# Kernel optimization log

Measured on AMD Instinct MI355X. Metric: run time of the kernel, lower is better.

The kernel has to match this reference:

```python
import jax, jax.numpy as jnp
import numpy as np

RSQRT2 = 2 ** (-0.5)
B, S, D_IN = 2, 4096, 1024
H, D_HEAD = 8, 64            # num_heads, attention_dim (per-head qk and v dim)
QK_DIM = H * D_HEAD          # 512
V_DIM = H * D_HEAD           # 512
OUT_DIM = D_IN               # 1024 (output_dim defaults to input_dim)
LN_EPS = 1e-5


def setup_inputs() -> dict:
    key = jax.random.key(0)
    ks = jax.random.split(key, 8)
    def lecun(k, fan_in, shape):
        return jax.random.normal(k, shape, dtype=jnp.float32) * (1.0 / np.sqrt(fan_in))
    return {
        "x": jax.random.normal(ks[0], (B, S, D_IN), dtype=jnp.float32),
        # weights stored [in, out] (transposed torch Linear layout)
        "W_qk": lecun(ks[1], D_IN, (D_IN, 2 * QK_DIM)),
        "b_qk": jnp.zeros((2 * QK_DIM,), jnp.float32),
        "W_v": lecun(ks[2], D_IN, (D_IN, V_DIM)),
        "b_v": jnp.zeros((V_DIM,), jnp.float32),
        "W_out": lecun(ks[3], V_DIM, (V_DIM, OUT_DIM)),
        "b_out": jnp.zeros((OUT_DIM,), jnp.float32),
        "ln_gamma": jnp.ones((OUT_DIM,), jnp.float32),
        "ln_beta": jnp.zeros((OUT_DIM,), jnp.float32),
    }


def _layernorm(y, gamma, beta):
    mu = jnp.mean(y, axis=-1, keepdims=True)
    var = jnp.mean(jnp.square(y - mu), axis=-1, keepdims=True)
    return (y - mu) * jax.lax.rsqrt(var + LN_EPS) * gamma + beta


def reference(x, W_qk, b_qk, W_v, b_v, W_out, b_out, ln_gamma, ln_beta):
    b, s, _ = x.shape
    scale = D_HEAD ** (-0.5)
    qk = x @ W_qk + b_qk                          # [b, s, 2*h*d]
    qk = qk.reshape(b, s, H, D_HEAD, 2)           # c (q/k) is fastest axis
    q, k = qk[..., 0], qk[..., 1]                 # [b, s, h, d]
    v = (x @ W_v + b_v).reshape(b, s, H, D_HEAD)  # [b, s, h, d]
    # manual multi-head attention, full O(s^2) score matrix (as in source)
    sim = jnp.einsum("bihd,bjhd->bhij", q, k) * scale
    attn = jax.nn.softmax(sim, axis=-1)           # [b, h, i, j]
    o = jnp.einsum("bhij,bjhd->bihd", attn, v)    # [b, s, h, d]
    o = o.reshape(b, s, V_DIM)                    # 'b h s d -> b s (h d)'
    y = _layernorm(o @ W_out + b_out, ln_gamma, ln_beta)
    return (y + x) * RSQRT2
```

## Files before the change

kernel.cpp:

```cpp
#include <hip/hip_runtime.h>
#include <stdint.h>

typedef short bf16x8 __attribute__((ext_vector_type(8)));
typedef float f32x4 __attribute__((ext_vector_type(4)));
typedef unsigned short ushort_t;

#define RSQRT2_F 0.70710678118654752440f
#define QSCALE_F 0.18033688011114382f

__device__ __forceinline__ ushort_t f2bf(float f) {
  union { float f; uint32_t u; } c; c.f = f;
  uint32_t u = c.u;
  uint32_t r = (u + 0x7fffu + ((u >> 16) & 1u)) >> 16;
  return (ushort_t)r;
}
__device__ __forceinline__ float bf2f(ushort_t u) {
  union { uint32_t u; float f; } c; c.u = ((uint32_t)u) << 16;
  return c.f;
}
__device__ __forceinline__ uint32_t fbits(float f) {
  union { float f; uint32_t u; } c; c.f = f; return c.u;
}

__device__ __forceinline__ void gload_lds16(const void* g, void* l) {
  __builtin_amdgcn_global_load_lds(
      (const __attribute__((address_space(1))) void*)g,
      (__attribute__((address_space(3))) void*)l, 16, 0, 0);
}

__global__ __launch_bounds__(256) void k_cvt_x(const float* __restrict__ x,
                                               ushort_t* __restrict__ xb) {
  int i = (blockIdx.x * 256 + threadIdx.x) * 4;
  float4 f = *(const float4*)(x + i);
  ushort4 o;
  o.x = f2bf(f.x); o.y = f2bf(f.y); o.z = f2bf(f.z); o.w = f2bf(f.w);
  *(ushort4*)(xb + i) = o;
}

__global__ __launch_bounds__(256) void k_build_wqkv(const float* __restrict__ Wqk,
                                                    const float* __restrict__ bqk,
                                                    const float* __restrict__ Wv,
                                                    const float* __restrict__ bv,
                                                    ushort_t* __restrict__ Wt,
                                                    float* __restrict__ biasAll) {
  int k = blockIdx.x * 256 + threadIdx.x;
  int n = blockIdx.y;
  float w, bb;
  if (n < 512)       { w = Wqk[(size_t)k * 1024 + 2 * n] * QSCALE_F;     bb = bqk[2 * n] * QSCALE_F; }
  else if (n < 1024) { w = Wqk[(size_t)k * 1024 + 2 * (n - 512) + 1];    bb = bqk[2 * (n - 512) + 1]; }
  else               { w = Wv[(size_t)k * 512 + (n - 1024)];             bb = bv[n - 1024]; }
  Wt[(size_t)n * 1024 + k] = f2bf(w);
  if (k == 0) biasAll[n] = bb;
}

__global__ __launch_bounds__(256) void k_build_wout(const float* __restrict__ Wout,
                                                    ushort_t* __restrict__ Wt) {
  int k = blockIdx.x * 256 + threadIdx.x;
  int n = blockIdx.y;
  Wt[(size_t)n * 512 + k] = f2bf(Wout[(size_t)k * 1024 + n]);
}

template <int MODE>
__global__ __launch_bounds__(256) void k_gemm_bt(
    const ushort_t* __restrict__ A, const ushort_t* __restrict__ Bt,
    const float* __restrict__ bias,
    ushort_t* __restrict__ out0, ushort_t* __restrict__ out1, ushort_t* __restrict__ out2,
    int M, int N, int K) {
  __shared__ __align__(16) ushort_t As[2][4][128][8];
  __shared__ __align__(16) ushort_t Bs[2][4][128][8];
  const int t = threadIdx.x;
  const int lane = t & 63;
  const int wave = t >> 6;

  const int nby = N >> 7;
  const int nwg = gridDim.x;
  const int xcd = blockIdx.x & 7, pos = blockIdx.x >> 3;
  const int swz = xcd * (nwg >> 3) + pos;
  const int bx = swz / nby, by = swz % nby;
  const int m0 = bx * 128, n0 = by * 128;

  const int wm = (wave >> 1) * 64, wn = (wave & 1) * 64;
  const int lg = lane >> 4, lr = lane & 15;

  const int srow = t & 127, sg = t >> 7;
  const ushort_t* gA = A + (size_t)(m0 + srow) * K + sg * 8;
  const ushort_t* gB = Bt + (size_t)(n0 + srow) * K + sg * 8;

  f32x4 acc[4][4] = {};

#define GEMM_STAGE(k0, bsel)                                   \
  do {                                                         \
    gload_lds16(gA + (k0), &As[bsel][sg][srow][0]);            \
    gload_lds16(gA + (k0) + 16, &As[bsel][sg + 2][srow][0]);   \
    gload_lds16(gB + (k0), &Bs[bsel][sg][srow][0]);            \
    gload_lds16(gB + (k0) + 16, &Bs[bsel][sg + 2][srow][0]);   \
  } while (0)

  GEMM_STAGE(0, 0);
  __syncthreads();
  int buf = 0;
  for (int k0 = 0; k0 < K; k0 += 32) {
    if (k0 + 32 < K) GEMM_STAGE(k0 + 32, buf ^ 1);
    bf16x8 af[4], bfr[4];
#pragma unroll
    for (int mi = 0; mi < 4; mi++) af[mi] = *(const bf16x8*)&As[buf][lg][wm + mi * 16 + lr][0];
#pragma unroll
    for (int ni = 0; ni < 4; ni++) bfr[ni] = *(const bf16x8*)&Bs[buf][lg][wn + ni * 16 + lr][0];
#pragma unroll
    for (int mi = 0; mi < 4; mi++)
#pragma unroll
      for (int ni = 0; ni < 4; ni++)
        acc[mi][ni] = __builtin_amdgcn_mfma_f32_16x16x32_bf16(af[mi], bfr[ni], acc[mi][ni], 0, 0, 0);
    __syncthreads();
    buf ^= 1;
  }
#undef GEMM_STAGE

#pragma unroll
  for (int mi = 0; mi < 4; mi++) {
    int rowb = m0 + wm + mi * 16 + (lane >> 4) * 4;
#pragma unroll
    for (int ni = 0; ni < 4; ni++) {
      int col = n0 + wn + ni * 16 + lr;
      float bc = bias[col];
#pragma unroll
      for (int reg = 0; reg < 4; reg++) {
        int row = rowb + reg;
        float v = acc[mi][ni][reg] + bc;
        if (MODE == 0) {
          if (col < 512) {
            out0[(size_t)row * 512 + col] = f2bf(v);
          } else if (col < 1024) {
            out1[(size_t)row * 512 + (col - 512)] = f2bf(v);
          } else {
            int hd = col - 1024;
            int bb = row >> 12, s = row & 4095;
            out2[((size_t)(bb << 9) + hd) * 4096 + s] = f2bf(v);
          }
        } else {
          out0[(size_t)row * 1024 + col] = f2bf(v);
        }
      }
    }
  }
}

__global__ __launch_bounds__(256, 2) void k_attn(const ushort_t* __restrict__ Qb,
                                                 const ushort_t* __restrict__ Kb,
                                                 const ushort_t* __restrict__ Vt,
                                                 ushort_t* __restrict__ Opart,
                                                 float* __restrict__ lpart) {
  __shared__ __align__(16) ushort_t Ks[2][8][64][8];
  __shared__ __align__(16) ushort_t Vs[2][8][64][8];
  __shared__ __align__(16) ushort_t Pl[4][4][1024];
  const int S = 4096;
  const int t = threadIdx.x, lane = t & 63, wave = t >> 6;
  const int lg = lane >> 4, lr = lane & 15;

  const int bid = blockIdx.x;
  const int xcd = bid & 7, idx = bid >> 3;
  const int bh = (xcd << 1) | (idx >> 5);
  const int rem = idx & 31;
  const int qb = rem >> 1;
  const int half = rem & 1;
  const int b = bh >> 3, h = bh & 7;
  const int qbase = qb * 256 + wave * 64;
  const int kvbase = half * 2048;

  bf16x8 qf[4][2];
#pragma unroll
  for (int su = 0; su < 4; su++) {
    const ushort_t* qp = Qb + ((size_t)(b * S + qbase + su * 16 + lr)) * 512 + h * 64 + lg * 8;
    qf[su][0] = *(const bf16x8*)qp;
    qf[su][1] = *(const bf16x8*)(qp + 32);
  }

  const int cj = t & 63, cg = t >> 6;
  const ushort_t* gK = Kb + ((size_t)b * S + cj) * 512 + h * 64 + cg * 8;
  const ushort_t* gV = Vt + ((size_t)bh * 64 + cj) * 4096 + cg * 8;

  const bf16x8 vones = {(short)0x3F80, (short)0x3F80, (short)0x3F80, (short)0x3F80,
                        (short)0x3F80, (short)0x3F80, (short)0x3F80, (short)0x3F80};

  int poff[4], pread[2];
#pragma unroll
  for (int nt = 0; nt < 4; nt++) poff[nt] = (lr * 128 + nt * 32 + lg * 8) ^ ((lr & 7) << 4);
#pragma unroll
  for (int kc = 0; kc < 2; kc++) pread[kc] = (lr * 128 + kc * 64 + lg * 16) ^ ((lr & 7) << 4);

  f32x4 of[4][4] = {};
  f32x4 of_sum[4] = {};

#define ATTN_STAGE(kv0, bsel)                                         \
  do {                                                                \
    gload_lds16(gK + (size_t)(kv0) * 512, &Ks[bsel][cg][cj][0]);      \
    gload_lds16(gK + (size_t)(kv0) * 512 + 32, &Ks[bsel][cg + 4][cj][0]); \
    gload_lds16(gV + (kv0), &Vs[bsel][cg][cj][0]);                    \
    gload_lds16(gV + (kv0) + 32, &Vs[bsel][cg + 4][cj][0]);           \
  } while (0)

  ATTN_STAGE(kvbase, 0);
  __syncthreads();
  int buf = 0;

  for (int kv0 = kvbase; kv0 < kvbase + 2048; kv0 += 64) {
    if (kv0 + 64 < kvbase + 2048) ATTN_STAGE(kv0 + 64, buf ^ 1);

    f32x4 sf[4][4];
    __builtin_amdgcn_s_setprio(1);
#pragma unroll
    for (int nt = 0; nt < 4; nt++) {
      bf16x8 kf0 = *(const bf16x8*)&Ks[buf][lg][nt * 16 + lr][0];
      bf16x8 kf1 = *(const bf16x8*)&Ks[buf][4 + lg][nt * 16 + lr][0];
#pragma unroll
      for (int su = 0; su < 4; su++) {
        f32x4 z = {};
        z = __builtin_amdgcn_mfma_f32_16x16x32_bf16(kf0, qf[su][0], z, 0, 0, 0);
        sf[su][nt] = __builtin_amdgcn_mfma_f32_16x16x32_bf16(kf1, qf[su][1], z, 0, 0, 0);
      }
    }
    __builtin_amdgcn_s_setprio(0);

    bf16x8 pf[4][2];
#pragma unroll
    for (int su = 0; su < 4; su++) {
      char* Pb = (char*)&Pl[wave][su][0];
#pragma unroll
      for (int nt = 0; nt < 4; nt++) {
        float p0 = __builtin_amdgcn_exp2f(sf[su][nt][0]);
        float p1 = __builtin_amdgcn_exp2f(sf[su][nt][1]);
        float p2 = __builtin_amdgcn_exp2f(sf[su][nt][2]);
        float p3 = __builtin_amdgcn_exp2f(sf[su][nt][3]);
        uint32_t w0 = (fbits(p0) >> 16) | (fbits(p1) & 0xffff0000u);
        uint32_t w1 = (fbits(p2) >> 16) | (fbits(p3) & 0xffff0000u);
        *(uint2*)(Pb + poff[nt]) = make_uint2(w0, w1);
      }
#pragma unroll
      for (int kc = 0; kc < 2; kc++) pf[su][kc] = *(const bf16x8*)(Pb + pread[kc]);
    }

    __builtin_amdgcn_s_setprio(1);
#pragma unroll
    for (int dt = 0; dt < 4; dt++) {
      bf16x8 vf0 = *(const bf16x8*)&Vs[buf][lg][dt * 16 + lr][0];
      bf16x8 vf1 = *(const bf16x8*)&Vs[buf][4 + lg][dt * 16 + lr][0];
#pragma unroll
      for (int su = 0; su < 4; su++) {
        of[su][dt] = __builtin_amdgcn_mfma_f32_16x16x32_bf16(pf[su][0], vf0, of[su][dt], 0, 0, 0);
        of[su][dt] = __builtin_amdgcn_mfma_f32_16x16x32_bf16(pf[su][1], vf1, of[su][dt], 0, 0, 0);
      }
    }
#pragma unroll
    for (int su = 0; su < 4; su++) {
      of_sum[su] = __builtin_amdgcn_mfma_f32_16x16x32_bf16(pf[su][0], vones, of_sum[su], 0, 0, 0);
      of_sum[su] = __builtin_amdgcn_mfma_f32_16x16x32_bf16(pf[su][1], vones, of_sum[su], 0, 0, 0);
    }
    __builtin_amdgcn_s_setprio(0);

    __syncthreads();
    buf ^= 1;
  }
#undef ATTN_STAGE

  ushort_t* Opw = Opart + ((size_t)half * 8192 + (size_t)b * 4096) * 512;
#pragma unroll
  for (int su = 0; su < 4; su++) {
#pragma unroll
    for (int dt = 0; dt < 4; dt++)
#pragma unroll
      for (int r = 0; r < 4; r++) {
        int q = qbase + su * 16 + lg * 4 + r;
        Opw[(size_t)q * 512 + h * 64 + dt * 16 + lr] = f2bf(of[su][dt][r]);
      }
    if (lr == 0) {
#pragma unroll
      for (int r = 0; r < 4; r++) {
        int q = qbase + su * 16 + lg * 4 + r;
        lpart[(((size_t)half * 2 + b) * 8 + h) * 4096 + q] = of_sum[su][r];
      }
    }
  }
}

__global__ __launch_bounds__(128) void k_merge(const ushort_t* __restrict__ Opart,
                                               const float* __restrict__ lpart,
                                               ushort_t* __restrict__ Ob) {
  const int row = blockIdx.x;
  const int t = threadIdx.x;
  const int col = t * 4;
  const int b = row >> 12, q = row & 4095;
  const int h = col >> 6;
  float l = lpart[(((size_t)0 * 2 + b) * 8 + h) * 4096 + q] +
            lpart[(((size_t)1 * 2 + b) * 8 + h) * 4096 + q];
  float inv = 1.0f / l;
  ushort4 a = *(const ushort4*)(Opart + (size_t)row * 512 + col);
  ushort4 c = *(const ushort4*)(Opart + ((size_t)8192 + row) * 512 + col);
  ushort4 o;
  o.x = f2bf((bf2f(a.x) + bf2f(c.x)) * inv);
  o.y = f2bf((bf2f(a.y) + bf2f(c.y)) * inv);
  o.z = f2bf((bf2f(a.z) + bf2f(c.z)) * inv);
  o.w = f2bf((bf2f(a.w) + bf2f(c.w)) * inv);
  *(ushort4*)(Ob + (size_t)row * 512 + col) = o;
}

__global__ __launch_bounds__(256) void k_ln(const ushort_t* __restrict__ ypre,
                                            const float* __restrict__ x,
                                            const float* __restrict__ gamma,
                                            const float* __restrict__ beta,
                                            float* __restrict__ out) {
  __shared__ float red[8];
  const int row = blockIdx.x, t = threadIdx.x;
  const ushort_t* yr = ypre + (size_t)row * 1024;
  ushort4 u = *(const ushort4*)(yr + t * 4);
  float v0 = bf2f(u.x), v1 = bf2f(u.y), v2 = bf2f(u.z), v3 = bf2f(u.w);
  float s = v0 + v1 + v2 + v3;
  float sq = v0 * v0 + v1 * v1 + v2 * v2 + v3 * v3;
#pragma unroll
  for (int m = 32; m; m >>= 1) { s += __shfl_xor(s, m, 64); sq += __shfl_xor(sq, m, 64); }
  if ((t & 63) == 0) { red[t >> 6] = s; red[4 + (t >> 6)] = sq; }
  __syncthreads();
  s = red[0] + red[1] + red[2] + red[3];
  sq = red[4] + red[5] + red[6] + red[7];
  float mu = s * (1.f / 1024.f);
  float var = sq * (1.f / 1024.f) - mu * mu;
  float inv = rsqrtf(var + 1e-5f);
  int c = t * 4;
  float4 xf = *(const float4*)(x + (size_t)row * 1024 + c);
  float4 o;
  o.x = ((v0 - mu) * inv * gamma[c + 0] + beta[c + 0] + xf.x) * RSQRT2_F;
  o.y = ((v1 - mu) * inv * gamma[c + 1] + beta[c + 1] + xf.y) * RSQRT2_F;
  o.z = ((v2 - mu) * inv * gamma[c + 2] + beta[c + 2] + xf.z) * RSQRT2_F;
  o.w = ((v3 - mu) * inv * gamma[c + 3] + beta[c + 3] + xf.w) * RSQRT2_F;
  *(float4*)(out + (size_t)row * 1024 + c) = o;
}

extern "C" void kernel_launch(void* const* d_in, const int* in_sizes, int n_in,
                              void* d_out, int out_size, void* d_ws, size_t ws_size,
                              hipStream_t stream) {
  (void)in_sizes; (void)n_in; (void)out_size; (void)ws_size;
  const float* x     = (const float*)d_in[0];
  const float* Wqk   = (const float*)d_in[1];
  const float* bqk   = (const float*)d_in[2];
  const float* Wv    = (const float*)d_in[3];
  const float* bv    = (const float*)d_in[4];
  const float* Wout  = (const float*)d_in[5];
  const float* bout  = (const float*)d_in[6];
  const float* gamma = (const float*)d_in[7];
  const float* beta  = (const float*)d_in[8];
  float* out = (float*)d_out;

  char* ws = (char*)d_ws;
  size_t off = 0;
  auto alloc = [&](size_t bytes) {
    off = (off + 255) & ~(size_t)255;
    void* p = ws + off;
    off += bytes;
    return p;
  };
  ushort_t* xb    = (ushort_t*)alloc(8192ull * 1024 * 2);
  ushort_t* Wqkvt = (ushort_t*)alloc(1536ull * 1024 * 2);
  float*    biasA = (float*)   alloc(1536ull * 4);
  ushort_t* Woutt = (ushort_t*)alloc(1024ull * 512 * 2);
  ushort_t* Qb    = (ushort_t*)alloc(8192ull * 512 * 2);
  ushort_t* Kbuf  = (ushort_t*)alloc(8192ull * 512 * 2);
  ushort_t* Vtb   = (ushort_t*)alloc(1024ull * 4096 * 2);
  ushort_t* Ob    = (ushort_t*)alloc(8192ull * 512 * 2);
  float*    lpart = (float*)   alloc(2ull * 2 * 8 * 4096 * 4);
  ushort_t* Opart = xb;
  ushort_t* ypre  = xb;

  k_cvt_x<<<8192, 256, 0, stream>>>(x, xb);
  k_build_wqkv<<<dim3(4, 1536), 256, 0, stream>>>(Wqk, bqk, Wv, bv, Wqkvt, biasA);
  k_build_wout<<<dim3(2, 1024), 256, 0, stream>>>(Wout, Woutt);
  k_gemm_bt<0><<<768, 256, 0, stream>>>(xb, Wqkvt, biasA, Qb, Kbuf, Vtb, 8192, 1536, 1024);
  k_attn<<<512, 256, 0, stream>>>(Qb, Kbuf, Vtb, Opart, lpart);
  k_merge<<<8192, 128, 0, stream>>>(Opart, lpart, Ob);
  k_gemm_bt<1><<<512, 256, 0, stream>>>(Ob, Woutt, bout, ypre, nullptr, nullptr, 8192, 1024, 512);
  k_ln<<<8192, 256, 0, stream>>>(ypre, x, gamma, beta, out);
}
```

Measured before the change: 207.3 us.

## Split attention KV range into quarters and raise occupancy to four blocks

The attention kernel now splits each query block's KV range into four 1024-key quarters instead of two halves, doubling the grid to 1024 blocks. The P staging buffer in LDS is shrunk to one slice per wave, and launch bounds ask for four blocks per CU. The merge kernel now sums four partial outputs and four row-sum partials, and buffers are reused to hold the extra partials. The goal is more parallelism and occupancy on the attention stage. In exchange, partial-output traffic and merge work double, and register pressure may rise under the tighter launch bound.

```diff
diff --git a/kernel.cpp b/kernel.cpp
--- a/kernel.cpp
+++ b/kernel.cpp
@@ -145,27 +145,30 @@
   }
 }
 
-__global__ __launch_bounds__(256, 2) void k_attn(const ushort_t* __restrict__ Qb,
+__global__ __launch_bounds__(256, 4) void k_attn(const ushort_t* __restrict__ Qb,
                                                  const ushort_t* __restrict__ Kb,
                                                  const ushort_t* __restrict__ Vt,
-                                                 ushort_t* __restrict__ Opart,
+                                                 ushort_t* __restrict__ O0,
+                                                 ushort_t* __restrict__ O1,
+                                                 ushort_t* __restrict__ O2,
+                                                 ushort_t* __restrict__ O3,
                                                  float* __restrict__ lpart) {
   __shared__ __align__(16) ushort_t Ks[2][8][64][8];
   __shared__ __align__(16) ushort_t Vs[2][8][64][8];
-  __shared__ __align__(16) ushort_t Pl[4][4][1024];
+  __shared__ __align__(16) ushort_t Pl[4][1024];
   const int S = 4096;
   const int t = threadIdx.x, lane = t & 63, wave = t >> 6;
   const int lg = lane >> 4, lr = lane & 15;
 
   const int bid = blockIdx.x;
   const int xcd = bid & 7, idx = bid >> 3;
-  const int bh = (xcd << 1) | (idx >> 5);
-  const int rem = idx & 31;
-  const int qb = rem >> 1;
-  const int half = rem & 1;
+  const int bh = (xcd << 1) | (idx >> 6);
+  const int rem = idx & 63;
+  const int qb = rem >> 2;
+  const int quarter = rem & 3;
   const int b = bh >> 3, h = bh & 7;
   const int qbase = qb * 256 + wave * 64;
-  const int kvbase = half * 2048;
+  const int kvbase = quarter * 1024;
 
   bf16x8 qf[4][2];
 #pragma unroll
@@ -203,8 +206,8 @@
   __syncthreads();
   int buf = 0;
 
-  for (int kv0 = kvbase; kv0 < kvbase + 2048; kv0 += 64) {
-    if (kv0 + 64 < kvbase + 2048) ATTN_STAGE(kv0 + 64, buf ^ 1);
+  for (int kv0 = kvbase; kv0 < kvbase + 1024; kv0 += 64) {
+    if (kv0 + 64 < kvbase + 1024) ATTN_STAGE(kv0 + 64, buf ^ 1);
 
     f32x4 sf[4][4];
     __builtin_amdgcn_s_setprio(1);
@@ -224,7 +227,7 @@
     bf16x8 pf[4][2];
 #pragma unroll
     for (int su = 0; su < 4; su++) {
-      char* Pb = (char*)&Pl[wave][su][0];
+      char* Pb = (char*)&Pl[wave][0];
 #pragma unroll
       for (int nt = 0; nt < 4; nt++) {
         float p0 = __builtin_amdgcn_exp2f(sf[su][nt][0]);
@@ -262,7 +265,8 @@
   }
 #undef ATTN_STAGE
 
-  ushort_t* Opw = Opart + ((size_t)half * 8192 + (size_t)b * 4096) * 512;
+  ushort_t* const opq[4] = {O0, O1, O2, O3};
+  ushort_t* Opw = opq[quarter] + (size_t)b * 4096 * 512;
 #pragma unroll
   for (int su = 0; su < 4; su++) {
 #pragma unroll
@@ -276,13 +280,16 @@
 #pragma unroll
       for (int r = 0; r < 4; r++) {
         int q = qbase + su * 16 + lg * 4 + r;
-        lpart[(((size_t)half * 2 + b) * 8 + h) * 4096 + q] = of_sum[su][r];
-      }
-    }
-  }
-}
-
-__global__ __launch_bounds__(128) void k_merge(const ushort_t* __restrict__ Opart,
+        lpart[(((size_t)quarter * 2 + b) * 8 + h) * 4096 + q] = of_sum[su][r];
+      }
+    }
+  }
+}
+
+__global__ __launch_bounds__(128) void k_merge(const ushort_t* __restrict__ O0,
+                                               const ushort_t* __restrict__ O1,
+                                               const ushort_t* __restrict__ O2,
+                                               const ushort_t* __restrict__ O3,
                                                const float* __restrict__ lpart,
                                                ushort_t* __restrict__ Ob) {
   const int row = blockIdx.x;
@@ -290,16 +297,20 @@
   const int col = t * 4;
   const int b = row >> 12, q = row & 4095;
   const int h = col >> 6;
-  float l = lpart[(((size_t)0 * 2 + b) * 8 + h) * 4096 + q] +
-            lpart[(((size_t)1 * 2 + b) * 8 + h) * 4096 + q];
+  float l = 0.f;
+#pragma unroll
+  for (int qu = 0; qu < 4; qu++)
+    l += lpart[(((size_t)qu * 2 + b) * 8 + h) * 4096 + q];
   float inv = 1.0f / l;
-  ushort4 a = *(const ushort4*)(Opart + (size_t)row * 512 + col);
-  ushort4 c = *(const ushort4*)(Opart + ((size_t)8192 + row) * 512 + col);
+  ushort4 a0 = *(const ushort4*)(O0 + (size_t)row * 512 + col);
+  ushort4 a1 = *(const ushort4*)(O1 + (size_t)row * 512 + col);
+  ushort4 a2 = *(const ushort4*)(O2 + (size_t)row * 512 + col);
+  ushort4 a3 = *(const ushort4*)(O3 + (size_t)row * 512 + col);
   ushort4 o;
-  o.x = f2bf((bf2f(a.x) + bf2f(c.x)) * inv);
-  o.y = f2bf((bf2f(a.y) + bf2f(c.y)) * inv);
-  o.z = f2bf((bf2f(a.z) + bf2f(c.z)) * inv);
-  o.w = f2bf((bf2f(a.w) + bf2f(c.w)) * inv);
+  o.x = f2bf((bf2f(a0.x) + bf2f(a1.x) + bf2f(a2.x) + bf2f(a3.x)) * inv);
+  o.y = f2bf((bf2f(a0.y) + bf2f(a1.y) + bf2f(a2.y) + bf2f(a3.y)) * inv);
+  o.z = f2bf((bf2f(a0.z) + bf2f(a1.z) + bf2f(a2.z) + bf2f(a3.z)) * inv);
+  o.w = f2bf((bf2f(a0.w) + bf2f(a1.w) + bf2f(a2.w) + bf2f(a3.w)) * inv);
   *(ushort4*)(Ob + (size_t)row * 512 + col) = o;
 }
 
@@ -364,17 +375,20 @@
   ushort_t* Qb    = (ushort_t*)alloc(8192ull * 512 * 2);
   ushort_t* Kbuf  = (ushort_t*)alloc(8192ull * 512 * 2);
   ushort_t* Vtb   = (ushort_t*)alloc(1024ull * 4096 * 2);
-  ushort_t* Ob    = (ushort_t*)alloc(8192ull * 512 * 2);
-  float*    lpart = (float*)   alloc(2ull * 2 * 8 * 4096 * 4);
-  ushort_t* Opart = xb;
+  ushort_t* Oq2   = (ushort_t*)alloc(8192ull * 512 * 2);
+  ushort_t* Oq3   = (ushort_t*)alloc(8192ull * 512 * 2);
+  float*    lpart = (float*)   alloc(4ull * 2 * 8 * 4096 * 4);
+  ushort_t* Oq0   = xb;
+  ushort_t* Oq1   = xb + 8192ull * 512;
+  ushort_t* Obm   = Qb;
   ushort_t* ypre  = xb;
 
   k_cvt_x<<<8192, 256, 0, stream>>>(x, xb);
   k_build_wqkv<<<dim3(4, 1536), 256, 0, stream>>>(Wqk, bqk, Wv, bv, Wqkvt, biasA);
   k_build_wout<<<dim3(2, 1024), 256, 0, stream>>>(Wout, Woutt);
   k_gemm_bt<0><<<768, 256, 0, stream>>>(xb, Wqkvt, biasA, Qb, Kbuf, Vtb, 8192, 1536, 1024);
-  k_attn<<<512, 256, 0, stream>>>(Qb, Kbuf, Vtb, Opart, lpart);
-  k_merge<<<8192, 128, 0, stream>>>(Opart, lpart, Ob);
-  k_gemm_bt<1><<<512, 256, 0, stream>>>(Ob, Woutt, bout, ypre, nullptr, nullptr, 8192, 1024, 512);
+  k_attn<<<1024, 256, 0, stream>>>(Qb, Kbuf, Vtb, Oq0, Oq1, Oq2, Oq3, lpart);
+  k_merge<<<8192, 128, 0, stream>>>(Oq0, Oq1, Oq2, Oq3, lpart, Obm);
+  k_gemm_bt<1><<<512, 256, 0, stream>>>(Obm, Woutt, bout, ypre, nullptr, nullptr, 8192, 1024, 512);
   k_ln<<<8192, 256, 0, stream>>>(ypre, x, gamma, beta, out);
 }
```

Result: slower. 486.4 us (+134.6%).
